# Kernel tuning notes

Hardware: AMD Instinct MI355X
Metric: run time of the kernel (lower is better)

The kernel has to match this reference:

```python
import jax, jax.numpy as jnp
import numpy as np


def setup_inputs() -> dict:
    key = jax.random.key(0)
    k1, k2, k3, k4 = jax.random.split(key, 4)
    B, N, L, D = 32, 64, 128, 256  # batch, max_node_num, max_node_len, d_model
    NB = B * N  # node batch
    src = jax.random.uniform(k1, (L, NB, 1), dtype=jnp.float32)
    memory_bank = jax.random.normal(k2, (L, NB, D), dtype=jnp.float32)
    lengths = jax.random.randint(k3, (NB,), 0, L, dtype=jnp.int32)
    recover = jax.random.permutation(k4, NB).astype(jnp.int32)
    return {
        "src": src,
        "memory_bank": memory_bank,
        "lengths": lengths,
        "recover": recover,
        "max_node_num": N,
        "max_node_len": L,
    }


def reference(src, memory_bank, lengths, recover, max_node_num, max_node_len):
    """Ragged node-batch -> original-batch reconstruction from NMTModel.forward.

    src:         [L, NB, 1] float  (L = max_node_len, NB = B * max_node_num)
    memory_bank: [L, NB, D] float  (encoder output, already in recovered order)
    lengths:     [NB] int          (per-node valid lengths, recovered order)
    recover:     [NB] int          (permutation applied to src only, as in torch)
    Returns (src_out [MAX_LEN,B,1], memory_bank_out [MAX_LEN,B,D],
             encoder_hidden [1,B,D], lengths_out [B]).
    """
    N, L = max_node_num, max_node_len
    NB = lengths.shape[0]
    B = NB // N
    D = memory_bank.shape[-1]
    MAX_LEN = N * L  # static upper bound on max(sum of lengths per batch item)

    # src.transpose(0,1)[recover].squeeze(-1) -> [NB, L], then group to [B, N, L]
    src_g = src[:, :, 0].T[recover].reshape(B, N, L)
    # memory_bank.transpose(0,1) -> [NB, L, D] grouped to [B, N, L, D]
    mb_g = jnp.transpose(memory_bank, (1, 0, 2)).reshape(B, N, L, D)

    len_bn = lengths.reshape(B, N)
    # exclusive prefix sum: start offset of each node's tokens inside its batch row
    off = jnp.cumsum(len_bn, axis=1) - len_bn  # [B, N]
    pos = jnp.arange(L)
    valid = pos[None, None, :] < len_bn[:, :, None]  # [B, N, L]
    dest = jnp.where(
        valid,
        jnp.arange(B)[:, None, None] * MAX_LEN + off[:, :, None] + pos[None, None, :],
        B * MAX_LEN,  # dummy slot for padded positions
    )
    df = dest.reshape(-1)

    # src_res initialized with ones (matches torch.ones), padded tail stays 1.0
    src_buf = jnp.ones(B * MAX_LEN + 1, dtype=src.dtype).at[df].set(src_g.reshape(-1))
    src_out = src_buf[:-1].reshape(B, MAX_LEN).T[:, :, None]  # [MAX_LEN, B, 1]

    # memory_bank_res initialized with zeros
    mb_buf = jnp.zeros((B * MAX_LEN + 1, D), dtype=memory_bank.dtype)
    mb_buf = mb_buf.at[df].set(mb_g.reshape(-1, D))
    mb_bt = mb_buf[:-1].reshape(B, MAX_LEN, D)
    memory_bank_out = jnp.transpose(mb_bt, (1, 0, 2))  # [MAX_LEN, B, D]

    lengths_out = len_bn.sum(axis=1).astype(jnp.float32)  # [B]

    # mean-pooled encoder state: mask / lengths, then bmm
    mask = (jnp.arange(MAX_LEN)[None, :] < lengths_out[:, None]).astype(mb_bt.dtype)
    mask = mask / lengths_out[:, None]
    encoder_hidden = jnp.einsum("bt,btd->bd", mask, mb_bt)[None]  # [1, B, D]

    return (src_out, memory_bank_out, encoder_hidden, lengths_out)
```

## Files before the change

kernel.cpp:

```cpp
#include <hip/hip_runtime.h>

#define BB 32
#define NN 64
#define LL 128
#define DD 256
#define NBTOT (BB * NN)
#define MAX_LEN (NN * LL)
#define D4 (DD / 4)

typedef float f32x4 __attribute__((ext_vector_type(4)));

__global__ __launch_bounds__(64) void prefix_kernel(
    const int* __restrict__ lengths,
    int* __restrict__ cum,
    float* __restrict__ inv_total,
    float* __restrict__ lengths_out,
    float* __restrict__ enc_hidden)
{
    const int b = blockIdx.x;
    const int lane = threadIdx.x;

    int v = lengths[b * NN + lane];
    #pragma unroll
    for (int s = 1; s < 64; s <<= 1) {
        int o = __shfl_up(v, s, 64);
        if (lane >= s) v += o;
    }
    cum[b * NN + lane] = v;

    const int total = __shfl(v, 63, 64);
    if (lane == 0) {
        lengths_out[b] = (float)total;
        inv_total[b] = (total > 0) ? (1.0f / (float)total) : 0.0f;
    }
    #pragma unroll
    for (int k = 0; k < DD / 64; ++k)
        enc_hidden[b * DD + k * 64 + lane] = 0.0f;
}

__global__ __launch_bounds__(256) void gather_kernel(
    const float* __restrict__ src,
    const f32x4* __restrict__ mb,
    const int* __restrict__ recover,
    const int* __restrict__ cum,
    const float* __restrict__ inv_total,
    float* __restrict__ src_out,
    f32x4* __restrict__ mb_out,
    float* __restrict__ enc_hidden)
{
    __shared__ int   s_cum[NN];
    __shared__ float s_accw[4][DD];

    const int b    = blockIdx.y;
    const int t0   = blockIdx.x * 256;
    const int tid  = threadIdx.x;
    const int wave = tid >> 6;
    const int lane = tid & 63;

    if (tid < NN) s_cum[tid] = cum[b * NN + tid];
    __syncthreads();

    const int total = s_cum[NN - 1];
    const int my_t  = t0 + tid;

    int n = 0;
    #pragma unroll
    for (int s = 32; s >= 1; s >>= 1) {
        const int cand = n + s;
        if (cand <= NN && s_cum[cand - 1] <= my_t) n = cand;
    }
    const int l = my_t - ((n > 0) ? s_cum[n - 1] : 0);

    const int rowidx = l * NBTOT + b * NN + n;

    float sv = 1.0f;
    if (my_t < total) sv = src[(size_t)l * NBTOT + recover[b * NN + n]];
    src_out[(size_t)my_t * BB + b] = sv;

    const int wbase = t0 + wave * 64;
    int nval = total - wbase;
    nval = nval < 0 ? 0 : (nval > 64 ? 64 : nval);

    f32x4 acc = {0.f, 0.f, 0.f, 0.f};

    int j = 0;
    #pragma unroll 4
    for (; j < nval; ++j) {
        const int r = __shfl(rowidx, j, 64);
        f32x4 v = __builtin_nontemporal_load(&mb[(size_t)r * D4 + lane]);
        acc += v;
        __builtin_nontemporal_store(
            v, &mb_out[((size_t)(wbase + j) * BB + b) * D4 + lane]);
    }
    const f32x4 z = {0.f, 0.f, 0.f, 0.f};
    #pragma unroll 8
    for (; j < 64; ++j) {
        __builtin_nontemporal_store(
            z, &mb_out[((size_t)(wbase + j) * BB + b) * D4 + lane]);
    }

    s_accw[wave][lane * 4 + 0] = acc.x;
    s_accw[wave][lane * 4 + 1] = acc.y;
    s_accw[wave][lane * 4 + 2] = acc.z;
    s_accw[wave][lane * 4 + 3] = acc.w;
    __syncthreads();

    const float partial = s_accw[0][tid] + s_accw[1][tid]
                        + s_accw[2][tid] + s_accw[3][tid];
    atomicAdd(&enc_hidden[b * DD + tid], partial * inv_total[b]);
}

extern "C" void kernel_launch(void* const* d_in, const int* in_sizes, int n_in,
                              void* d_out, int out_size, void* d_ws, size_t ws_size,
                              hipStream_t stream) {
    const float* src     = (const float*)d_in[0];
    const float* mb      = (const float*)d_in[1];
    const int*   lengths = (const int*)d_in[2];
    const int*   recover = (const int*)d_in[3];

    float* out = (float*)d_out;
    float* src_out     = out;
    float* mb_out      = out + (size_t)MAX_LEN * BB;
    float* enc_hidden  = mb_out + (size_t)MAX_LEN * BB * DD;
    float* lengths_out = enc_hidden + (size_t)BB * DD;

    int*   cum       = (int*)d_ws;
    float* inv_total = (float*)((char*)d_ws + NBTOT * sizeof(int));

    prefix_kernel<<<BB, 64, 0, stream>>>(lengths, cum, inv_total,
                                         lengths_out, enc_hidden);

    dim3 grid(MAX_LEN / 256, BB);
    gather_kernel<<<grid, 256, 0, stream>>>(src, (const f32x4*)mb, recover,
                                            cum, inv_total,
                                            src_out, (f32x4*)mb_out,
                                            enc_hidden);
}
```

Baseline: 422.2 us.

## Remap gather to contiguous output rows with shared-memory reduction and slotted partial sums

Each block now covers 256 consecutive output rows (interleaved t,b), so mb_out stores form one contiguous stream instead of rows spaced BB*D apart. Loads are batched eight at a time to keep more memory requests in flight. Per-batch sums go through shared-memory atomics into a 32 KB per-block buffer. They are then flushed with global atomics into 8 slots per element, and a new finalize kernel reduces the slots and scales by 1/length. This adds LDS atomic traffic, a large shared allocation that lowers occupancy, and an extra kernel launch.

```diff
diff --git a/kernel.cpp b/kernel.cpp
--- a/kernel.cpp
+++ b/kernel.cpp
@@ -7,6 +7,7 @@
 #define NBTOT (BB * NN)
 #define MAX_LEN (NN * LL)
 #define D4 (DD / 4)
+#define NSLOT 8
 
 typedef float f32x4 __attribute__((ext_vector_type(4)));
 
@@ -15,7 +16,7 @@
     int* __restrict__ cum,
     float* __restrict__ inv_total,
     float* __restrict__ lengths_out,
-    float* __restrict__ enc_hidden)
+    float* __restrict__ ws_part)
 {
     const int b = blockIdx.x;
     const int lane = threadIdx.x;
@@ -33,9 +34,11 @@
         lengths_out[b] = (float)total;
         inv_total[b] = (total > 0) ? (1.0f / (float)total) : 0.0f;
     }
+
+    const int tg = b * 64 + lane;
     #pragma unroll
-    for (int k = 0; k < DD / 64; ++k)
-        enc_hidden[b * DD + k * 64 + lane] = 0.0f;
+    for (int k = 0; k < (BB * DD * NSLOT) / (BB * 64); ++k)
+        ws_part[k * (BB * 64) + tg] = 0.0f;
 }
 
 __global__ __launch_bounds__(256) void gather_kernel(
@@ -43,71 +46,109 @@
     const f32x4* __restrict__ mb,
     const int* __restrict__ recover,
     const int* __restrict__ cum,
-    const float* __restrict__ inv_total,
     float* __restrict__ src_out,
     f32x4* __restrict__ mb_out,
-    float* __restrict__ enc_hidden)
+    float* __restrict__ ws_part)
 {
-    __shared__ int   s_cum[NN];
-    __shared__ float s_accw[4][DD];
+    __shared__ int   s_cum[BB][NN + 1];
+    __shared__ float s_acc[BB * DD];
+    __shared__ int   s_any;
 
-    const int b    = blockIdx.y;
-    const int t0   = blockIdx.x * 256;
     const int tid  = threadIdx.x;
     const int wave = tid >> 6;
     const int lane = tid & 63;
+    const int r0   = blockIdx.x * 256;
+    const int t0   = r0 >> 5;
 
-    if (tid < NN) s_cum[tid] = cum[b * NN + tid];
+    for (int k = tid; k < BB * NN; k += 256)
+        s_cum[k >> 6][k & 63] = cum[k];
+    for (int k = tid; k < BB * DD; k += 256)
+        s_acc[k] = 0.0f;
+    if (tid == 0) s_any = 0;
     __syncthreads();
 
-    const int total = s_cum[NN - 1];
-    const int my_t  = t0 + tid;
+    const int r = r0 + tid;
+    const int b = tid & 31;
+    const int t = r >> 5;
+    const int total = s_cum[b][NN - 1];
+    const bool valid = (t < total);
 
     int n = 0;
     #pragma unroll
     for (int s = 32; s >= 1; s >>= 1) {
         const int cand = n + s;
-        if (cand <= NN && s_cum[cand - 1] <= my_t) n = cand;
+        if (cand <= NN && s_cum[b][cand - 1] <= t) n = cand;
     }
-    const int l = my_t - ((n > 0) ? s_cum[n - 1] : 0);
-
+    const int l = t - ((n > 0) ? s_cum[b][n - 1] : 0);
     const int rowidx = l * NBTOT + b * NN + n;
 
+    if (valid) s_any = 1;
+
     float sv = 1.0f;
-    if (my_t < total) sv = src[(size_t)l * NBTOT + recover[b * NN + n]];
-    src_out[(size_t)my_t * BB + b] = sv;
+    if (valid) sv = src[(size_t)l * NBTOT + recover[b * NN + n]];
+    src_out[r] = sv;
 
-    const int wbase = t0 + wave * 64;
-    int nval = total - wbase;
-    nval = nval < 0 ? 0 : (nval > 64 ? 64 : nval);
+    const unsigned long long vmask = __ballot(valid);
 
-    f32x4 acc = {0.f, 0.f, 0.f, 0.f};
+    const int rw = r0 + wave * 64;
+    f32x4* const outp = mb_out + (size_t)rw * D4 + lane;
+    const f32x4 z = {0.f, 0.f, 0.f, 0.f};
 
-    int j = 0;
-    #pragma unroll 4
-    for (; j < nval; ++j) {
-        const int r = __shfl(rowidx, j, 64);
-        f32x4 v = __builtin_nontemporal_load(&mb[(size_t)r * D4 + lane]);
-        acc += v;
-        __builtin_nontemporal_store(
-            v, &mb_out[((size_t)(wbase + j) * BB + b) * D4 + lane]);
-    }
-    const f32x4 z = {0.f, 0.f, 0.f, 0.f};
-    #pragma unroll 8
-    for (; j < 64; ++j) {
-        __builtin_nontemporal_store(
-            z, &mb_out[((size_t)(wbase + j) * BB + b) * D4 + lane]);
+    for (int jb = 0; jb < 8; ++jb) {
+        int   rj[8];
+        f32x4 v[8];
+        #pragma unroll
+        for (int k = 0; k < 8; ++k)
+            rj[k] = __shfl(rowidx, jb * 8 + k, 64);
+        #pragma unroll
+        for (int k = 0; k < 8; ++k) {
+            const int j = jb * 8 + k;
+            if ((vmask >> j) & 1)
+                v[k] = __builtin_nontemporal_load(&mb[(size_t)rj[k] * D4 + lane]);
+            else
+                v[k] = z;
+        }
+        #pragma unroll
+        for (int k = 0; k < 8; ++k) {
+            const int j = jb * 8 + k;
+            __builtin_nontemporal_store(v[k], outp + (size_t)j * D4);
+            if ((vmask >> j) & 1) {
+                const int bj = (rw + j) & 31;
+                float* const ap = &s_acc[bj * DD];
+                atomicAdd(ap + 0 * 64 + lane, v[k].x);
+                atomicAdd(ap + 1 * 64 + lane, v[k].y);
+                atomicAdd(ap + 2 * 64 + lane, v[k].z);
+                atomicAdd(ap + 3 * 64 + lane, v[k].w);
+            }
+        }
     }
 
-    s_accw[wave][lane * 4 + 0] = acc.x;
-    s_accw[wave][lane * 4 + 1] = acc.y;
-    s_accw[wave][lane * 4 + 2] = acc.z;
-    s_accw[wave][lane * 4 + 3] = acc.w;
     __syncthreads();
+    if (s_any) {
+        const int slot = blockIdx.x & (NSLOT - 1);
+        #pragma unroll 4
+        for (int b2 = 0; b2 < BB; ++b2) {
+            if (s_cum[b2][NN - 1] > t0) {
+                const float pv = s_acc[b2 * DD + tid];
+                atomicAdd(&ws_part[(b2 * DD + tid) * NSLOT + slot], pv);
+            }
+        }
+    }
+}
 
-    const float partial = s_accw[0][tid] + s_accw[1][tid]
-                        + s_accw[2][tid] + s_accw[3][tid];
-    atomicAdd(&enc_hidden[b * DD + tid], partial * inv_total[b]);
+__global__ __launch_bounds__(256) void finalize_kernel(
+    const float* __restrict__ ws_part,
+    const float* __restrict__ inv_total,
+    float* __restrict__ enc_hidden)
+{
+    const int b = blockIdx.x;
+    const int c = threadIdx.x;
+    const int p = (c & 3) * 64 + (c >> 2);
+    float s = 0.0f;
+    #pragma unroll
+    for (int k = 0; k < NSLOT; ++k)
+        s += ws_part[(b * DD + p) * NSLOT + k];
+    enc_hidden[b * DD + c] = s * inv_total[b];
 }
 
 extern "C" void kernel_launch(void* const* d_in, const int* in_sizes, int n_in,
@@ -126,13 +167,14 @@
 
     int*   cum       = (int*)d_ws;
     float* inv_total = (float*)((char*)d_ws + NBTOT * sizeof(int));
+    float* ws_part   = (float*)((char*)d_ws + 16384);
 
     prefix_kernel<<<BB, 64, 0, stream>>>(lengths, cum, inv_total,
-                                         lengths_out, enc_hidden);
+                                         lengths_out, ws_part);
 
-    dim3 grid(MAX_LEN / 256, BB);
-    gather_kernel<<<grid, 256, 0, stream>>>(src, (const f32x4*)mb, recover,
-                                            cum, inv_total,
-                                            src_out, (f32x4*)mb_out,
-                                            enc_hidden);
+    gather_kernel<<<(MAX_LEN * BB) / 256, 256, 0, stream>>>(
+        src, (const f32x4*)mb, recover, cum,
+        src_out, (f32x4*)mb_out, ws_part);
+
+    finalize_kernel<<<BB, 256, 0, stream>>>(ws_part, inv_total, enc_hidden);
 }
```

Measured after the change: 645.4 us. 52.9% more time.
